# Kernel optimization log

Measured on AMD Instinct MI355X. Metric: run time of the kernel, lower is better.

The kernel has to match this reference:

```python
import jax, jax.numpy as jnp
import numpy as np

B, N, DIM = 4, 1024, 2048
H, HKV, D = 16, 4, 128          # n_heads, n_kv_heads, head_dim
CACHE = 3072                     # cached KV length
WINDOW = 2048                    # max_window_len (sliding window)
EPS = 1e-6


def setup_inputs() -> dict:
    key = jax.random.key(0)
    ks = jax.random.split(key, 10)
    x = jax.random.normal(ks[0], (B, N, DIM), dtype=jnp.float32)
    past_k = jax.random.normal(ks[1], (B, HKV, CACHE, D), dtype=jnp.float32)
    past_v = jax.random.normal(ks[2], (B, HKV, CACHE, D), dtype=jnp.float32)
    # RoPE angles for the current segment (absolute positions CACHE..CACHE+N-1),
    # matching MultiLevelRoPE 'face' level: freqs = 1/theta**(arange(0,D,2)/D)
    pos = jnp.arange(CACHE, CACHE + N, dtype=jnp.float32)
    inv_freq = 1.0 / (10000.0 ** (jnp.arange(0, D, 2, dtype=jnp.float32) / D))
    ang = pos[:, None] * inv_freq[None, :]          # [N, D//2]
    freqs_cos = jnp.cos(ang)
    freqs_sin = jnp.sin(ang)
    s = 0.02
    Wq = jax.random.normal(ks[3], (H * D, DIM), dtype=jnp.float32) * s
    Wk = jax.random.normal(ks[4], (HKV * D, DIM), dtype=jnp.float32) * s
    Wv = jax.random.normal(ks[5], (HKV * D, DIM), dtype=jnp.float32) * s
    Wo = jax.random.normal(ks[6], (DIM, H * D), dtype=jnp.float32) * s
    bo = jnp.zeros((DIM,), dtype=jnp.float32)
    wq_norm = jnp.ones((D,), dtype=jnp.float32)
    wk_norm = jnp.ones((D,), dtype=jnp.float32)
    return {"x": x, "past_k": past_k, "past_v": past_v,
            "freqs_cos": freqs_cos, "freqs_sin": freqs_sin,
            "Wq": Wq, "Wk": Wk, "Wv": Wv, "Wo": Wo, "bo": bo,
            "wq_norm": wq_norm, "wk_norm": wk_norm}


def _rms_norm(t, w):
    # torch.nn.RMSNorm over head_dim
    return t * jax.lax.rsqrt(jnp.mean(t * t, axis=-1, keepdims=True) + EPS) * w


def _rope(t, cos, sin):
    # interleaved-pair complex rotation, as in MultiLevelRoPE.apply
    # t: [B, h, N, D]; cos/sin: [N, D//2]
    t2 = t.reshape(*t.shape[:-1], D // 2, 2)
    x0, x1 = t2[..., 0], t2[..., 1]
    c = cos[None, None, :, :]
    s = sin[None, None, :, :]
    r0 = x0 * c - x1 * s
    r1 = x0 * s + x1 * c
    return jnp.stack([r0, r1], axis=-1).reshape(t.shape)


def reference(x, past_k, past_v, freqs_cos, freqs_sin,
              Wq, Wk, Wv, Wo, bo, wq_norm, wk_norm):
    # projections -> [B, h, N, D]
    q = (x @ Wq.T).reshape(B, N, H, D).transpose(0, 2, 1, 3)
    k = (x @ Wk.T).reshape(B, N, HKV, D).transpose(0, 2, 1, 3)
    v = (x @ Wv.T).reshape(B, N, HKV, D).transpose(0, 2, 1, 3)
    # qk rms_norm on head_dim
    q = _rms_norm(q, wq_norm)
    k = _rms_norm(k, wk_norm)
    # RoPE on current segment (cached K already rotated)
    q = _rope(q, freqs_cos, freqs_sin)
    k = _rope(k, freqs_cos, freqs_sin)
    # append to cache -> M = CACHE + N
    k_all = jnp.concatenate([past_k, k], axis=2)   # [B, HKV, M, D]
    v_all = jnp.concatenate([past_v, v], axis=2)
    # repeat_kv for GQA
    n_rep = H // HKV
    k_rep = jnp.repeat(k_all, n_rep, axis=1)       # [B, H, M, D]
    v_rep = jnp.repeat(v_all, n_rep, axis=1)
    M = CACHE + N
    scale = 1.0 / jnp.sqrt(jnp.asarray(D, dtype=q.dtype))
    scores = jnp.einsum('bhnd,bhmd->bhnm', q, k_rep) * scale
    # causal + sliding-window mask over absolute positions
    qpos = jnp.arange(N) + CACHE                   # [N]
    kpos = jnp.arange(M)                           # [M]
    allowed = (kpos[None, :] <= qpos[:, None]) & (qpos[:, None] - kpos[None, :] < WINDOW)
    scores = jnp.where(allowed[None, None], scores, jnp.asarray(-1e30, dtype=scores.dtype))
    probs = jax.nn.softmax(scores, axis=-1)
    attn = jnp.einsum('bhnm,bhmd->bhnd', probs, v_rep)
    attn = attn.transpose(0, 2, 1, 3).reshape(B, N, H * D)
    return attn @ Wo.T + bo
```

## Files before the change

kernel.cpp:

```cpp
#include <hip/hip_runtime.h>
#include <hip/hip_bf16.h>
#include <stdint.h>

typedef unsigned short u16;
typedef unsigned int u32;
typedef __attribute__((ext_vector_type(8))) __bf16 bfrag;
typedef __attribute__((ext_vector_type(4))) float f32x4;
typedef __attribute__((ext_vector_type(16))) float f32x16;
typedef __attribute__((ext_vector_type(4))) unsigned short u16x4;

__device__ __forceinline__ u16 f2bf(float f){
  union { float f; u32 u; } v; v.f = f;
  u32 u = v.u;
  return (u16)((u + 0x7fffu + ((u >> 16) & 1u)) >> 16);
}

__device__ __forceinline__ u32 cvtpk(float a, float b){
  u32 r; asm("v_cvt_pk_bf16_f32 %0, %1, %2" : "=v"(r) : "v"(a), "v"(b)); return r;
}
__device__ __forceinline__ void swap32(u32 &a, u32 &b){
  asm volatile("v_permlane32_swap_b32 %0, %1" : "+v"(a), "+v"(b));
}

__device__ __forceinline__ void gload_lds16(const void* g, void* l){
  __builtin_amdgcn_global_load_lds(
      (__attribute__((address_space(1))) void*)(unsigned long long)g,
      (__attribute__((address_space(3))) void*)(u32)(unsigned long long)l,
      16, 0, 0);
}

__global__ void __launch_bounds__(256) k_cvt(const float* __restrict__ s, u16* __restrict__ d, int n4){
  int i = blockIdx.x*256 + threadIdx.x;
  if (i >= n4) return;
  float4 v = ((const float4*)s)[i];
  u16x4 o; o[0]=f2bf(v.x); o[1]=f2bf(v.y); o[2]=f2bf(v.z); o[3]=f2bf(v.w);
  ((u16x4*)d)[i] = o;
}

__global__ void __launch_bounds__(256) k_cvt_past(const float* __restrict__ s, u16* __restrict__ d, int n4){
  int i = blockIdx.x*256 + threadIdx.x;
  if (i >= n4) return;
  int e = i*4;
  int row = e >> 7;
  int col = e & 127;
  int bh = row / 3072;
  int m = row - bh*3072;
  float4 v = ((const float4*)s)[i];
  u16x4 o; o[0]=f2bf(v.x); o[1]=f2bf(v.y); o[2]=f2bf(v.z); o[3]=f2bf(v.w);
  *(u16x4*)(d + ((size_t)(bh*4096 + m) << 7) + col) = o;
}

__global__ void __launch_bounds__(256) k_cvt_past_vt(const float* __restrict__ s, u16* __restrict__ v_t){
  __shared__ u16 T[64][65];
  const int mt = blockIdx.x, dt = blockIdx.y, pl = blockIdx.z;
  const float* src = s + (size_t)pl*3072*128 + (size_t)mt*64*128 + dt*64;
  u16* dst = v_t + (size_t)pl*128*4096 + (size_t)dt*64*4096 + mt*64;
  const int t = threadIdx.x;
  #pragma unroll
  for (int r = 0; r < 2; ++r){
    int row = r*32 + (t >> 3);
    int c8 = (t & 7)*8;
    float4 va = *(const float4*)(src + (size_t)row*128 + c8);
    float4 vb = *(const float4*)(src + (size_t)row*128 + c8 + 4);
    T[row][c8+0]=f2bf(va.x); T[row][c8+1]=f2bf(va.y); T[row][c8+2]=f2bf(va.z); T[row][c8+3]=f2bf(va.w);
    T[row][c8+4]=f2bf(vb.x); T[row][c8+5]=f2bf(vb.y); T[row][c8+6]=f2bf(vb.z); T[row][c8+7]=f2bf(vb.w);
  }
  __syncthreads();
  #pragma unroll
  for (int r = 0; r < 2; ++r){
    int drow = r*32 + (t >> 3);
    int m8 = (t & 7)*8;
    union { bfrag v; u16 e[8]; } uv;
    #pragma unroll
    for (int j = 0; j < 8; ++j) uv.e[j] = T[m8 + j][drow];
    *(bfrag*)(dst + (size_t)drow*4096 + m8) = uv.v;
  }
}

template<int EPI>
__global__ void __launch_bounds__(256) k_gemm(
    const u16* __restrict__ A, const u16* __restrict__ Bm,
    u16* __restrict__ Cb, float* __restrict__ Cf, const float* __restrict__ bias,
    int M, int Nn, int K)
{
  __shared__ u16 lsA[2][4096];
  __shared__ u16 lsB[2][4096];
  const int t = threadIdx.x, lane = t & 63, wid = t >> 6;
  const int l15 = lane & 15, l4 = lane >> 4;
  const int wm = wid >> 1, wn = wid & 1;
  const int bn = blockIdx.x, bm = blockIdx.y;
  const u16* Ab = A + (size_t)bm*128*K;
  const u16* Bb = Bm + (size_t)bn*128*K;

  auto stage = [&](u16* ls, const u16* g, int kof){
    #pragma unroll
    for (int r = 0; r < 2; ++r){
      int row = r*64 + (t >> 2);
      int s = (t & 3) ^ ((row >> 1) & 3);
      gload_lds16(g + (size_t)row*K + kof + s*8, ls + r*2048 + wid*512);
    }
  };

  f32x4 acc[4][4] = {};
  stage(&lsA[0][0], Ab, 0);
  stage(&lsB[0][0], Bb, 0);
  const int NT = K >> 5;
  const int sl = l4 ^ ((l15 >> 1) & 3);
  const int ra0 = wm*64 + l15, rb0 = wn*64 + l15;
  for (int kt = 0; kt < NT; ++kt){
    __syncthreads();
    const int cur = kt & 1;
    if (kt + 1 < NT){
      stage(&lsA[cur ^ 1][0], Ab, (kt + 1)*32);
      stage(&lsB[cur ^ 1][0], Bb, (kt + 1)*32);
    }
    bfrag af[4], bfv[4];
    #pragma unroll
    for (int i = 0; i < 4; ++i){
      af[i]  = *(const bfrag*)&lsA[cur][(ra0 + i*16)*32 + sl*8];
      bfv[i] = *(const bfrag*)&lsB[cur][(rb0 + i*16)*32 + sl*8];
    }
    #pragma unroll
    for (int i = 0; i < 4; ++i)
      #pragma unroll
      for (int j = 0; j < 4; ++j)
        acc[i][j] = __builtin_amdgcn_mfma_f32_16x16x32_bf16(af[i], bfv[j], acc[i][j], 0, 0, 0);
  }
  const int row0 = bm*128 + wm*64, col0 = bn*128 + wn*64;
  #pragma unroll
  for (int i = 0; i < 4; ++i)
    #pragma unroll
    for (int j = 0; j < 4; ++j){
      int cc = col0 + j*16 + l15;
      float bv = (EPI == 1) ? bias[cc] : 0.f;
      #pragma unroll
      for (int r = 0; r < 4; ++r){
        int rr = row0 + i*16 + l4*4 + r;
        if (EPI == 0) Cb[(size_t)rr*Nn + cc] = f2bf(acc[i][j][r]);
        else          Cf[(size_t)rr*Nn + cc] = acc[i][j][r] + bv;
      }
    }
}

__global__ void __launch_bounds__(256) k_rmsrope(
    const u16* __restrict__ proj, const float* __restrict__ cosb, const float* __restrict__ sinb,
    const float* __restrict__ wq, const float* __restrict__ wk,
    u16* __restrict__ q_ro, u16* __restrict__ k_all, u16* __restrict__ v_all)
{
  const int bn = blockIdx.x;
  const int b = bn >> 10, n = bn & 1023;
  const int lane = threadIdx.x & 63, w = threadIdx.x >> 6;
  const int chunk = blockIdx.y*4 + w;
  const u16* src = proj + (size_t)bn*3072 + chunk*128 + lane*2;
  const u32 raw = *(const u32*)src;
  union { u32 u; float f; } a, c2;
  a.u = raw << 16; c2.u = raw & 0xffff0000u;
  float x0 = a.f, x1 = c2.f;
  if (chunk >= 20){
    int hk = chunk - 20;
    *(u32*)(v_all + (((size_t)(b*4 + hk)*4096 + 3072 + n) << 7) + lane*2) = raw;
    return;
  }
  float ss = x0*x0 + x1*x1;
  #pragma unroll
  for (int m = 1; m < 64; m <<= 1) ss += __shfl_xor(ss, m, 64);
  float inv = rsqrtf(ss*(1.f/128.f) + 1e-6f);
  const float* wn2 = (chunk < 16) ? wq : wk;
  x0 *= inv*wn2[lane*2]; x1 *= inv*wn2[lane*2 + 1];
  float cz = cosb[n*64 + lane], sz = sinb[n*64 + lane];
  float r0 = x0*cz - x1*sz;
  float r1 = x0*sz + x1*cz;
  u32 outp = (u32)f2bf(r0) | ((u32)f2bf(r1) << 16);
  if (chunk < 16){
    *(u32*)(q_ro + (((size_t)(b*16 + chunk)*1024 + n) << 7) + lane*2) = outp;
  } else {
    int hk = chunk - 16;
    *(u32*)(k_all + (((size_t)(b*4 + hk)*4096 + 3072 + n) << 7) + lane*2) = outp;
  }
}

__global__ void __launch_bounds__(256) k_transpose_v(const u16* __restrict__ v_all, u16* __restrict__ v_t){
  __shared__ u16 T[64][65];
  const int mt = blockIdx.x + 48, dt = blockIdx.y, pl = blockIdx.z;
  const u16* src = v_all + (size_t)pl*4096*128 + (size_t)mt*64*128 + dt*64;
  u16* dst = v_t + (size_t)pl*128*4096 + (size_t)dt*64*4096 + mt*64;
  const int t = threadIdx.x;
  #pragma unroll
  for (int r = 0; r < 2; ++r){
    int row = r*32 + (t >> 3);
    int c8 = (t & 7)*8;
    bfrag v = *(const bfrag*)(src + (size_t)row*128 + c8);
    union { bfrag v; u16 e[8]; } uv; uv.v = v;
    #pragma unroll
    for (int j = 0; j < 8; ++j) T[row][c8 + j] = uv.e[j];
  }
  __syncthreads();
  #pragma unroll
  for (int r = 0; r < 2; ++r){
    int drow = r*32 + (t >> 3);
    int m8 = (t & 7)*8;
    union { bfrag v; u16 e[8]; } uv;
    #pragma unroll
    for (int j = 0; j < 8; ++j) uv.e[j] = T[m8 + j][drow];
    *(bfrag*)(dst + (size_t)drow*4096 + m8) = uv.v;
  }
}

__global__ void __launch_bounds__(256, 2) k_attn(
    const u16* __restrict__ q_ro, const u16* __restrict__ k_all,
    const u16* __restrict__ v_t, u16* __restrict__ attn_o)
{
  __shared__ u16 Kl[2][64*128];
  __shared__ u16 Vt[2][128*64];
  const int bid = blockIdx.x;
  const int xcd = bid & 7, idx = bid >> 3;
  const int plane = (xcd << 1) | (idx >> 5);
  const int qt = idx & 31;
  const int b = plane >> 2, hk = plane & 3;
  const int t = threadIdx.x, lane = t & 63, w = t >> 6;
  const int l31 = lane & 31, lh = lane >> 5;
  const int h = hk*4 + w;
  const int qbase = qt*32;

  const u16* qplane = q_ro + (size_t)(b*16 + h)*1024*128;
  const u16* kplane = k_all + (size_t)(b*4 + hk)*4096*128;
  const u16* vplane = v_t  + (size_t)(b*4 + hk)*128*4096;

  bfrag qf[8];
  {
    const u16* qrow = qplane + (size_t)(qbase + l31)*128 + lh*8;
    #pragma unroll
    for (int dks = 0; dks < 8; ++dks)
      qf[dks] = *(const bfrag*)(qrow + dks*16);
  }

  auto stage = [&](int buf, int kb){
    #pragma unroll
    for (int r = 0; r < 4; ++r){
      int row = r*16 + (t >> 4);
      int scol = ((t & 15) ^ (row & 7) ^ ((row & 8) ? 8 : 0) ^ ((row & 8) ? 8 : 0)) * 8;
      gload_lds16(kplane + (size_t)(kb + row)*128 + (((t & 15) ^ (row & 7))*8), &Kl[buf][r*2048 + t*8]);
      (void)scol;
    }
    #pragma unroll
    for (int r = 0; r < 4; ++r){
      int row = r*32 + (t >> 3);
      gload_lds16(vplane + (size_t)row*4096 + kb + (((t & 7) ^ (row & 7))*8), &Vt[buf][r*2048 + t*8]);
    }
  };

  f32x16 acc_o[4] = {};
  float m_run = -1e30f, l_run = 0.f;
  const float KL = 0.127529904f;
  const int kb0 = (qbase + 1024) & ~63;
  const int qpos = 3072 + qbase + l31;

  stage(0, kb0);
  int cur = 0;
  for (int c = 0; c < 33; ++c){
    __syncthreads();
    const int kb = kb0 + c*64;
    if (c < 32) stage(cur ^ 1, kb + 64);

    f32x16 s0 = {}, s1 = {};
    #pragma unroll
    for (int dks = 0; dks < 8; ++dks){
      const int sw = l31 & 7;
      bfrag k0 = *(const bfrag*)&Kl[cur][(l31)*128      + (((dks*2 + lh) ^ sw)*8)];
      bfrag k1 = *(const bfrag*)&Kl[cur][(32 + l31)*128 + (((dks*2 + lh) ^ sw)*8)];
      s0 = __builtin_amdgcn_mfma_f32_32x32x16_bf16(k0, qf[dks], s0, 0, 0, 0);
      s1 = __builtin_amdgcn_mfma_f32_32x32x16_bf16(k1, qf[dks], s1, 0, 0, 0);
    }

    if ((c == 0) | (c == 32)){
      #pragma unroll
      for (int r = 0; r < 16; ++r){
        int krow = (r & 3) + 8*(r >> 2) + 4*lh;
        int d0 = qpos - (kb + krow);
        int d1 = qpos - (kb + 32 + krow);
        if ((unsigned)d0 >= 2048u) s0[r] = -1e30f;
        if ((unsigned)d1 >= 2048u) s1[r] = -1e30f;
      }
    }

    float mx = s0[0];
    #pragma unroll
    for (int r = 1; r < 16; ++r) mx = fmaxf(mx, s0[r]);
    #pragma unroll
    for (int r = 0; r < 16; ++r) mx = fmaxf(mx, s1[r]);
    mx = fmaxf(mx, __shfl_xor(mx, 32, 64));

    if (__any(mx > m_run + 62.7f)){
      float mnew = fmaxf(m_run, mx);
      float ef = exp2f(KL*(m_run - mnew));
      m_run = mnew;
      l_run *= ef;
      #pragma unroll
      for (int dj = 0; dj < 4; ++dj)
        #pragma unroll
        for (int r = 0; r < 16; ++r) acc_o[dj][r] *= ef;
    }
    const float nKm = -KL*m_run;
    float ls = 0.f;
    #pragma unroll
    for (int r = 0; r < 16; ++r){ float p = exp2f(fmaf(KL, s0[r], nKm)); s0[r] = p; ls += p; }
    #pragma unroll
    for (int r = 0; r < 16; ++r){ float p = exp2f(fmaf(KL, s1[r], nKm)); s1[r] = p; ls += p; }
    l_run += ls;

    union { u32 u[4]; bfrag v; } pfrag[4];
    {
      u32 a0 = cvtpk(s0[0],  s0[1]),  a1 = cvtpk(s0[2],  s0[3]);
      u32 b0 = cvtpk(s0[4],  s0[5]),  b1 = cvtpk(s0[6],  s0[7]);
      swap32(a0, b0); swap32(a1, b1);
      pfrag[0].u[0]=a0; pfrag[0].u[1]=a1; pfrag[0].u[2]=b0; pfrag[0].u[3]=b1;
      u32 c0 = cvtpk(s0[8],  s0[9]),  c1 = cvtpk(s0[10], s0[11]);
      u32 e0 = cvtpk(s0[12], s0[13]), e1 = cvtpk(s0[14], s0[15]);
      swap32(c0, e0); swap32(c1, e1);
      pfrag[1].u[0]=c0; pfrag[1].u[1]=c1; pfrag[1].u[2]=e0; pfrag[1].u[3]=e1;
    }
    {
      u32 a0 = cvtpk(s1[0],  s1[1]),  a1 = cvtpk(s1[2],  s1[3]);
      u32 b0 = cvtpk(s1[4],  s1[5]),  b1 = cvtpk(s1[6],  s1[7]);
      swap32(a0, b0); swap32(a1, b1);
      pfrag[2].u[0]=a0; pfrag[2].u[1]=a1; pfrag[2].u[2]=b0; pfrag[2].u[3]=b1;
      u32 c0 = cvtpk(s1[8],  s1[9]),  c1 = cvtpk(s1[10], s1[11]);
      u32 e0 = cvtpk(s1[12], s1[13]), e1 = cvtpk(s1[14], s1[15]);
      swap32(c0, e0); swap32(c1, e1);
      pfrag[3].u[0]=c0; pfrag[3].u[1]=c1; pfrag[3].u[2]=e0; pfrag[3].u[3]=e1;
    }

    #pragma unroll
    for (int ks = 0; ks < 4; ++ks)
      #pragma unroll
      for (int dj = 0; dj < 4; ++dj){
        int row = dj*32 + l31;
        bfrag vf = *(const bfrag*)&Vt[cur][row*64 + (((ks*2 + lh) ^ (row & 7))*8)];
        acc_o[dj] = __builtin_amdgcn_mfma_f32_32x32x16_bf16(vf, pfrag[ks].v, acc_o[dj], 0, 0, 0);
      }
    cur ^= 1;
  }

  float lt = l_run + __shfl_xor(l_run, 32, 64);
  float inv = 1.0f / lt;
  const int bn = b*1024 + qbase + l31;
  u16* orow = attn_o + (size_t)bn*2048 + h*128;
  #pragma unroll
  for (int dj = 0; dj < 4; ++dj)
    #pragma unroll
    for (int rg = 0; rg < 4; ++rg){
      int d0 = dj*32 + rg*8 + 4*lh;
      u16x4 o;
      #pragma unroll
      for (int r2 = 0; r2 < 4; ++r2) o[r2] = f2bf(acc_o[dj][rg*4 + r2]*inv);
      *(u16x4*)(orow + d0) = o;
    }
}

extern "C" void kernel_launch(void* const* d_in, const int* in_sizes, int n_in,
                              void* d_out, int out_size, void* d_ws, size_t ws_size,
                              hipStream_t stream)
{
  const float* x      = (const float*)d_in[0];
  const float* past_k = (const float*)d_in[1];
  const float* past_v = (const float*)d_in[2];
  const float* fcos   = (const float*)d_in[3];
  const float* fsin   = (const float*)d_in[4];
  const float* Wq     = (const float*)d_in[5];
  const float* Wk     = (const float*)d_in[6];
  const float* Wv     = (const float*)d_in[7];
  const float* Wo     = (const float*)d_in[8];
  const float* bo     = (const float*)d_in[9];
  const float* wqn    = (const float*)d_in[10];
  const float* wkn    = (const float*)d_in[11];
  float* out = (float*)d_out;
  char* ws = (char*)d_ws;

  u16* xb    = (u16*)(ws);
  u16* wqkv  = (u16*)(ws + 16777216);
  u16* wo_b  = (u16*)(ws + 29360128);
  u16* q_ro  = (u16*)(ws + 37748736);
  u16* k_all = (u16*)(ws + 54525952);
  u16* v_all = (u16*)(ws + 71303168);
  u16* v_t   = (u16*)(ws + 88080384);
  u16* proj  = (u16*)(ws + 104857600);
  u16* attn_o = proj;

  k_cvt<<<8192, 256, 0, stream>>>(x, xb, 2097152);
  k_cvt<<<4096, 256, 0, stream>>>(Wq, wqkv, 1048576);
  k_cvt<<<1024, 256, 0, stream>>>(Wk, wqkv + 2048*2048, 262144);
  k_cvt<<<1024, 256, 0, stream>>>(Wv, wqkv + 2560*2048, 262144);
  k_cvt<<<4096, 256, 0, stream>>>(Wo, wo_b, 1048576);
  k_cvt_past<<<6144, 256, 0, stream>>>(past_k, k_all, 1572864);
  k_cvt_past_vt<<<dim3(48, 2, 16), 256, 0, stream>>>(past_v, v_t);

  k_gemm<0><<<dim3(24, 32), 256, 0, stream>>>(xb, wqkv, proj, nullptr, nullptr, 4096, 3072, 2048);
  k_rmsrope<<<dim3(4096, 6), 256, 0, stream>>>(proj, fcos, fsin, wqn, wkn, q_ro, k_all, v_all);
  k_transpose_v<<<dim3(16, 2, 16), 256, 0, stream>>>(v_all, v_t);
  k_attn<<<512, 256, 0, stream>>>(q_ro, k_all, v_t, attn_o);
  k_gemm<1><<<dim3(16, 32), 256, 0, stream>>>(attn_o, wo_b, nullptr, out, bo, 4096, 2048, 2048);
}
```

Baseline: 257.4 us.

## Split key tiles across two wave groups and drop online-max rescaling in attention

The attention kernel grows to 512 threads. Two groups of four waves each take one 32-key half of every 64-key tile, and their partial outputs and row sums are merged through LDS at the end. The softmax scale and log2e factor are folded into Q during the RMSNorm/RoPE pass. The running-max tracking and accumulator rescaling are removed, which relies on RMS-normalised Q and K keeping the scores small enough that exp2 cannot overflow. This cuts per-wave MFMA and softmax work and raises parallelism, but overflow safety now depends on the norm weights staying modest, and the final merge adds extra LDS traffic and a barrier.

```diff
diff --git a/kernel.cpp b/kernel.cpp
--- a/kernel.cpp
+++ b/kernel.cpp
@@ -170,11 +170,14 @@
   float cz = cosb[n*64 + lane], sz = sinb[n*64 + lane];
   float r0 = x0*cz - x1*sz;
   float r1 = x0*sz + x1*cz;
-  u32 outp = (u32)f2bf(r0) | ((u32)f2bf(r1) << 16);
   if (chunk < 16){
+    const float KLF = 0.127529904f;
+    r0 *= KLF; r1 *= KLF;
+    u32 outp = (u32)f2bf(r0) | ((u32)f2bf(r1) << 16);
     *(u32*)(q_ro + (((size_t)(b*16 + chunk)*1024 + n) << 7) + lane*2) = outp;
   } else {
     int hk = chunk - 16;
+    u32 outp = (u32)f2bf(r0) | ((u32)f2bf(r1) << 16);
     *(u32*)(k_all + (((size_t)(b*4 + hk)*4096 + 3072 + n) << 7) + lane*2) = outp;
   }
 }
@@ -206,12 +209,12 @@
   }
 }
 
-__global__ void __launch_bounds__(256, 2) k_attn(
+__global__ void __launch_bounds__(512, 4) k_attn(
     const u16* __restrict__ q_ro, const u16* __restrict__ k_all,
     const u16* __restrict__ v_t, u16* __restrict__ attn_o)
 {
-  __shared__ u16 Kl[2][64*128];
-  __shared__ u16 Vt[2][128*64];
+  __shared__ u16 smem[32768];
+  __shared__ float Lsh[4][32];
   const int bid = blockIdx.x;
   const int xcd = bid & 7, idx = bid >> 3;
   const int plane = (xcd << 1) | (idx >> 5);
@@ -219,7 +222,9 @@
   const int b = plane >> 2, hk = plane & 3;
   const int t = threadIdx.x, lane = t & 63, w = t >> 6;
   const int l31 = lane & 31, lh = lane >> 5;
-  const int h = hk*4 + w;
+  const int hf = w >> 2;
+  const int hd = w & 3;
+  const int h = hk*4 + hd;
   const int qbase = qt*32;
 
   const u16* qplane = q_ro + (size_t)(b*16 + h)*1024*128;
@@ -234,127 +239,138 @@
       qf[dks] = *(const bfrag*)(qrow + dks*16);
   }
 
-  auto stage = [&](int buf, int kb){
-    #pragma unroll
-    for (int r = 0; r < 4; ++r){
-      int row = r*16 + (t >> 4);
-      int scol = ((t & 15) ^ (row & 7) ^ ((row & 8) ? 8 : 0) ^ ((row & 8) ? 8 : 0)) * 8;
-      gload_lds16(kplane + (size_t)(kb + row)*128 + (((t & 15) ^ (row & 7))*8), &Kl[buf][r*2048 + t*8]);
-      (void)scol;
-    }
-    #pragma unroll
-    for (int r = 0; r < 4; ++r){
-      int row = r*32 + (t >> 3);
-      gload_lds16(vplane + (size_t)row*4096 + kb + (((t & 7) ^ (row & 7))*8), &Vt[buf][r*2048 + t*8]);
-    }
-  };
-
-  f32x16 acc_o[4] = {};
-  float m_run = -1e30f, l_run = 0.f;
-  const float KL = 0.127529904f;
+  const int krow = t >> 4, kslot = t & 15;
+  const int koff0 = krow*128 + ((kslot ^ (krow & 7))*8);
+  const int vrow = t >> 3, vslot = t & 7;
+  const int voff0 = vrow*4096 + ((vslot ^ (vrow & 7))*8);
+
+  const int swb = (lh << 4) ^ ((l31 & 7) << 4);
+  const int kaddr = (hf*32 + l31)*256 + swb;
+  const int vaddr = l31*128 + swb;
+
   const int kb0 = (qbase + 1024) & ~63;
   const int qpos = 3072 + qbase + l31;
-
-  stage(0, kb0);
-  int cur = 0;
+  const char* smb = (const char*)smem;
+
+  f32x16 acc_o[4] = {};
+  float l_run = 0.f;
+
+  {
+    const u16* kc = kplane + (size_t)kb0*128;
+    const u16* vc = vplane + kb0;
+    gload_lds16(kc + koff0,          smem + t*8);
+    gload_lds16(kc + koff0 + 4096,   smem + 4096 + t*8);
+    gload_lds16(vc + voff0,          smem + 16384 + t*8);
+    gload_lds16(vc + voff0 + 262144, smem + 20480 + t*8);
+  }
+
   for (int c = 0; c < 33; ++c){
     __syncthreads();
-    const int kb = kb0 + c*64;
-    if (c < 32) stage(cur ^ 1, kb + 64);
-
-    f32x16 s0 = {}, s1 = {};
+    const int cur = c & 1;
+    if (c < 32){
+      const u16* kc = kplane + (size_t)(kb0 + (c + 1)*64)*128;
+      const u16* vc = vplane + kb0 + (c + 1)*64;
+      u16* kd = smem + (cur ^ 1)*8192;
+      u16* vd = smem + 16384 + (cur ^ 1)*8192;
+      gload_lds16(kc + koff0,          kd + t*8);
+      gload_lds16(kc + koff0 + 4096,   kd + 4096 + t*8);
+      gload_lds16(vc + voff0,          vd + t*8);
+      gload_lds16(vc + voff0 + 262144, vd + 4096 + t*8);
+    }
+
+    const int kaddrB = kaddr + cur*16384;
+    const int vaddrB = vaddr + cur*16384;
+
+    f32x16 s = {};
+    __builtin_amdgcn_s_setprio(1);
     #pragma unroll
     for (int dks = 0; dks < 8; ++dks){
-      const int sw = l31 & 7;
-      bfrag k0 = *(const bfrag*)&Kl[cur][(l31)*128      + (((dks*2 + lh) ^ sw)*8)];
-      bfrag k1 = *(const bfrag*)&Kl[cur][(32 + l31)*128 + (((dks*2 + lh) ^ sw)*8)];
-      s0 = __builtin_amdgcn_mfma_f32_32x32x16_bf16(k0, qf[dks], s0, 0, 0, 0);
-      s1 = __builtin_amdgcn_mfma_f32_32x32x16_bf16(k1, qf[dks], s1, 0, 0, 0);
-    }
+      bfrag kf = *(const bfrag*)(smb + (kaddrB ^ (dks << 5)));
+      s = __builtin_amdgcn_mfma_f32_32x32x16_bf16(kf, qf[dks], s, 0, 0, 0);
+    }
+    __builtin_amdgcn_s_setprio(0);
 
     if ((c == 0) | (c == 32)){
+      const int kb = kb0 + c*64;
       #pragma unroll
       for (int r = 0; r < 16; ++r){
-        int krow = (r & 3) + 8*(r >> 2) + 4*lh;
-        int d0 = qpos - (kb + krow);
-        int d1 = qpos - (kb + 32 + krow);
-        if ((unsigned)d0 >= 2048u) s0[r] = -1e30f;
-        if ((unsigned)d1 >= 2048u) s1[r] = -1e30f;
+        int kpos = kb + hf*32 + (r & 3) + 8*(r >> 2) + 4*lh;
+        int dq = qpos - kpos;
+        if ((unsigned)dq >= 2048u) s[r] = -1e30f;
       }
     }
 
-    float mx = s0[0];
-    #pragma unroll
-    for (int r = 1; r < 16; ++r) mx = fmaxf(mx, s0[r]);
-    #pragma unroll
-    for (int r = 0; r < 16; ++r) mx = fmaxf(mx, s1[r]);
-    mx = fmaxf(mx, __shfl_xor(mx, 32, 64));
-
-    if (__any(mx > m_run + 62.7f)){
-      float mnew = fmaxf(m_run, mx);
-      float ef = exp2f(KL*(m_run - mnew));
-      m_run = mnew;
-      l_run *= ef;
-      #pragma unroll
-      for (int dj = 0; dj < 4; ++dj)
+    #pragma unroll
+    for (int r = 0; r < 16; ++r) s[r] = exp2f(s[r]);
+    {
+      float a0 = (s[0]+s[1]) + (s[2]+s[3]);
+      float a1 = (s[4]+s[5]) + (s[6]+s[7]);
+      float a2 = (s[8]+s[9]) + (s[10]+s[11]);
+      float a3 = (s[12]+s[13]) + (s[14]+s[15]);
+      float lc = (a0 + a1) + (a2 + a3);
+      lc += __shfl_xor(lc, 32, 64);
+      l_run += lc;
+    }
+
+    union { u32 u[4]; bfrag v; } pf[2];
+    {
+      u32 a0 = cvtpk(s[0],  s[1]),  a1 = cvtpk(s[2],  s[3]);
+      u32 b0 = cvtpk(s[4],  s[5]),  b1 = cvtpk(s[6],  s[7]);
+      swap32(a0, b0); swap32(a1, b1);
+      pf[0].u[0]=a0; pf[0].u[1]=a1; pf[0].u[2]=b0; pf[0].u[3]=b1;
+      u32 c0 = cvtpk(s[8],  s[9]),  c1 = cvtpk(s[10], s[11]);
+      u32 e0 = cvtpk(s[12], s[13]), e1 = cvtpk(s[14], s[15]);
+      swap32(c0, e0); swap32(c1, e1);
+      pf[1].u[0]=c0; pf[1].u[1]=c1; pf[1].u[2]=e0; pf[1].u[3]=e1;
+    }
+
+    __builtin_amdgcn_s_setprio(1);
+    #pragma unroll
+    for (int lks = 0; lks < 2; ++lks){
+      const int va = vaddrB ^ ((hf*2 + lks) << 5);
+      #pragma unroll
+      for (int dj = 0; dj < 4; ++dj){
+        bfrag vf = *(const bfrag*)(smb + 32768 + va + dj*4096);
+        acc_o[dj] = __builtin_amdgcn_mfma_f32_32x32x16_bf16(vf, pf[lks].v, acc_o[dj], 0, 0, 0);
+      }
+    }
+    __builtin_amdgcn_s_setprio(0);
+  }
+
+  __syncthreads();
+  float* Om = (float*)smem;
+  if (hf == 1){
+    if (lh == 0) Lsh[hd][l31] = l_run;
+    #pragma unroll
+    for (int dj = 0; dj < 4; ++dj)
+      #pragma unroll
+      for (int rg = 0; rg < 4; ++rg){
+        int slot = dj*8 + rg*2 + lh;
+        f32x4 vv;
         #pragma unroll
-        for (int r = 0; r < 16; ++r) acc_o[dj][r] *= ef;
-    }
-    const float nKm = -KL*m_run;
-    float ls = 0.f;
-    #pragma unroll
-    for (int r = 0; r < 16; ++r){ float p = exp2f(fmaf(KL, s0[r], nKm)); s0[r] = p; ls += p; }
-    #pragma unroll
-    for (int r = 0; r < 16; ++r){ float p = exp2f(fmaf(KL, s1[r], nKm)); s1[r] = p; ls += p; }
-    l_run += ls;
-
-    union { u32 u[4]; bfrag v; } pfrag[4];
-    {
-      u32 a0 = cvtpk(s0[0],  s0[1]),  a1 = cvtpk(s0[2],  s0[3]);
-      u32 b0 = cvtpk(s0[4],  s0[5]),  b1 = cvtpk(s0[6],  s0[7]);
-      swap32(a0, b0); swap32(a1, b1);
-      pfrag[0].u[0]=a0; pfrag[0].u[1]=a1; pfrag[0].u[2]=b0; pfrag[0].u[3]=b1;
-      u32 c0 = cvtpk(s0[8],  s0[9]),  c1 = cvtpk(s0[10], s0[11]);
-      u32 e0 = cvtpk(s0[12], s0[13]), e1 = cvtpk(s0[14], s0[15]);
-      swap32(c0, e0); swap32(c1, e1);
-      pfrag[1].u[0]=c0; pfrag[1].u[1]=c1; pfrag[1].u[2]=e0; pfrag[1].u[3]=e1;
-    }
-    {
-      u32 a0 = cvtpk(s1[0],  s1[1]),  a1 = cvtpk(s1[2],  s1[3]);
-      u32 b0 = cvtpk(s1[4],  s1[5]),  b1 = cvtpk(s1[6],  s1[7]);
-      swap32(a0, b0); swap32(a1, b1);
-      pfrag[2].u[0]=a0; pfrag[2].u[1]=a1; pfrag[2].u[2]=b0; pfrag[2].u[3]=b1;
-      u32 c0 = cvtpk(s1[8],  s1[9]),  c1 = cvtpk(s1[10], s1[11]);
-      u32 e0 = cvtpk(s1[12], s1[13]), e1 = cvtpk(s1[14], s1[15]);
-      swap32(c0, e0); swap32(c1, e1);
-      pfrag[3].u[0]=c0; pfrag[3].u[1]=c1; pfrag[3].u[2]=e0; pfrag[3].u[3]=e1;
-    }
-
-    #pragma unroll
-    for (int ks = 0; ks < 4; ++ks)
-      #pragma unroll
-      for (int dj = 0; dj < 4; ++dj){
-        int row = dj*32 + l31;
-        bfrag vf = *(const bfrag*)&Vt[cur][row*64 + (((ks*2 + lh) ^ (row & 7))*8)];
-        acc_o[dj] = __builtin_amdgcn_mfma_f32_32x32x16_bf16(vf, pfrag[ks].v, acc_o[dj], 0, 0, 0);
+        for (int j = 0; j < 4; ++j) vv[j] = acc_o[dj][rg*4 + j];
+        *(f32x4*)&Om[hd*4096 + l31*128 + ((slot ^ (l31 & 7)) << 2)] = vv;
       }
-    cur ^= 1;
-  }
-
-  float lt = l_run + __shfl_xor(l_run, 32, 64);
-  float inv = 1.0f / lt;
-  const int bn = b*1024 + qbase + l31;
-  u16* orow = attn_o + (size_t)bn*2048 + h*128;
-  #pragma unroll
-  for (int dj = 0; dj < 4; ++dj)
-    #pragma unroll
-    for (int rg = 0; rg < 4; ++rg){
-      int d0 = dj*32 + rg*8 + 4*lh;
-      u16x4 o;
-      #pragma unroll
-      for (int r2 = 0; r2 < 4; ++r2) o[r2] = f2bf(acc_o[dj][rg*4 + r2]*inv);
-      *(u16x4*)(orow + d0) = o;
-    }
+  }
+  __syncthreads();
+  if (hf == 0){
+    float ltot = l_run + Lsh[hd][l31];
+    float inv = 1.0f / ltot;
+    const int bn = b*1024 + qbase + l31;
+    u16* orow = attn_o + (size_t)bn*2048 + h*128;
+    #pragma unroll
+    for (int dj = 0; dj < 4; ++dj)
+      #pragma unroll
+      for (int rg = 0; rg < 4; ++rg){
+        int slot = dj*8 + rg*2 + lh;
+        f32x4 vv = *(const f32x4*)&Om[hd*4096 + l31*128 + ((slot ^ (l31 & 7)) << 2)];
+        int d0 = dj*32 + rg*8 + lh*4;
+        u16x4 o;
+        #pragma unroll
+        for (int j = 0; j < 4; ++j) o[j] = f2bf((acc_o[dj][rg*4 + j] + vv[j])*inv);
+        *(u16x4*)(orow + d0) = o;
+      }
+  }
 }
 
 extern "C" void kernel_launch(void* const* d_in, const int* in_sizes, int n_in,
@@ -397,6 +413,6 @@
   k_gemm<0><<<dim3(24, 32), 256, 0, stream>>>(xb, wqkv, proj, nullptr, nullptr, 4096, 3072, 2048);
   k_rmsrope<<<dim3(4096, 6), 256, 0, stream>>>(proj, fcos, fsin, wqn, wkn, q_ro, k_all, v_all);
   k_transpose_v<<<dim3(16, 2, 16), 256, 0, stream>>>(v_all, v_t);
-  k_attn<<<512, 256, 0, stream>>>(q_ro, k_all, v_t, attn_o);
+  k_attn<<<512, 512, 0, stream>>>(q_ro, k_all, v_t, attn_o);
   k_gemm<1><<<dim3(16, 32), 256, 0, stream>>>(attn_o, wo_b, nullptr, out, bo, 4096, 2048, 2048);
 }
```

Result: slower. 265.7 us (+3.2%).
